# Kernel optimization log

Hardware: AMD Instinct MI355X
Metric: run time of the kernel (lower is better)

Reference implementation:

```python
import jax, jax.numpy as jnp
import numpy as np

B, S1, S2 = 32, 128, 128
V, D, P, C = 30000, 300, 200, 3


def _highway(x, Wh, bh, Wt, bt):
    h = jax.nn.relu(x @ Wh + bh)
    t = jax.nn.sigmoid(x @ Wt + bt)
    return t * h + (1.0 - t) * x


def _ff(x, W1, b1, W2, b2):
    # self.forward: two relu linear layers (dropout disabled / keep_prob=1)
    return jax.nn.relu(jax.nn.relu(x @ W1 + b1) @ W2 + b2)


def setup_inputs() -> dict:
    key = jax.random.key(0)
    ks = iter(jax.random.split(key, 64))
    W = lambda *s: jax.random.normal(next(ks), s, jnp.float32) * 0.05
    Z = lambda n: jnp.zeros((n,), jnp.float32)
    inp = {
        'x1': jax.random.randint(next(ks), (B, S1), 0, V),
        'x2': jax.random.randint(next(ks), (B, S2), 0, V),
        'emb': jax.random.normal(next(ks), (V, D), jnp.float32),
        'hw1_Wh': W(D, D), 'hw1_bh': Z(D), 'hw1_Wt': W(D, D), 'hw1_bt': Z(D),
        'hw2_Wh': W(D, D), 'hw2_bh': Z(D), 'hw2_Wt': W(D, D), 'hw2_bt': Z(D),
        'mul_W1': W(D, P), 'mul_b1': Z(P), 'mul_W2': W(P, P), 'mul_b2': Z(P),
        'dist_W1': W(D, P), 'dist_b1': Z(P), 'dist_W2': W(P, P), 'dist_b2': Z(P),
        'cmp_W1': W(4 * D, P), 'cmp_b1': Z(P), 'cmp_W2': W(P, P), 'cmp_b2': Z(P),
        'chw1_Wh': W(P, P), 'chw1_bh': Z(P), 'chw1_Wt': W(P, P), 'chw1_bt': Z(P),
        'chw2_Wh': W(P, P), 'chw2_bh': Z(P), 'chw2_Wt': W(P, P), 'chw2_bt': Z(P),
        'agg_W1': W(4 * P, P), 'agg_b1': Z(P), 'agg_W2': W(P, P), 'agg_b2': Z(P),
        'out_W': W(P, C), 'out_b': Z(C),
    }
    return inp


def reference(x1, x2, emb,
              hw1_Wh, hw1_bh, hw1_Wt, hw1_bt,
              hw2_Wh, hw2_bh, hw2_Wt, hw2_bt,
              mul_W1, mul_b1, mul_W2, mul_b2,
              dist_W1, dist_b1, dist_W2, dist_b2,
              cmp_W1, cmp_b1, cmp_W2, cmp_b2,
              chw1_Wh, chw1_bh, chw1_Wt, chw1_bt,
              chw2_Wh, chw2_bh, chw2_Wt, chw2_bt,
              agg_W1, agg_b1, agg_W2, agg_b2,
              out_W, out_b):
    # embed + shared highway stack
    e1 = emb[x1]  # [B,S1,D]
    e2 = emb[x2]  # [B,S2,D]
    e1 = _highway(_highway(e1, hw1_Wh, hw1_bh, hw1_Wt, hw1_bt), hw2_Wh, hw2_bh, hw2_Wt, hw2_bt)
    e2 = _highway(_highway(e2, hw1_Wh, hw1_bh, hw1_Wt, hw1_bt), hw2_Wh, hw2_bh, hw2_Wt, hw2_bt)

    # attention_mul: project both, dot product
    p1 = _ff(e1, mul_W1, mul_b1, mul_W2, mul_b2)  # [B,S1,P]
    p2 = _ff(e2, mul_W1, mul_b1, mul_W2, mul_b2)  # [B,S2,P]
    att1 = jnp.einsum('bip,bjp->bij', p1, p2)

    # attention_dist: project both, sum_d 1/(1+|q1-q2|) -> 4D broadcast
    q1 = _ff(e1, dist_W1, dist_b1, dist_W2, dist_b2)
    q2 = _ff(e2, dist_W1, dist_b1, dist_W2, dist_b2)
    att2 = jnp.sum(1.0 / (1.0 + jnp.abs(q1[:, :, None, :] - q2[:, None, :, :])), axis=-1)

    sim = att1 + att2  # [B,S1,S2]
    alpha = jnp.einsum('bji,bjd->bid', jax.nn.softmax(jnp.swapaxes(sim, 1, 2), axis=-1).transpose(0, 2, 1).transpose(0, 2, 1), e1) if False else jnp.matmul(jax.nn.softmax(jnp.swapaxes(sim, 1, 2), axis=-1), e1)  # [B,S2,D]
    beta = jnp.matmul(jax.nn.softmax(sim, axis=-1), e2)  # [B,S1,D]

    # compare (shared forward + highway stack)
    v1 = _ff(jnp.concatenate([e1, beta, e1 - beta, e1 * beta], -1), cmp_W1, cmp_b1, cmp_W2, cmp_b2)
    v2 = _ff(jnp.concatenate([e2, alpha, e2 - alpha, e2 * alpha], -1), cmp_W1, cmp_b1, cmp_W2, cmp_b2)
    v1 = _highway(_highway(v1, chw1_Wh, chw1_bh, chw1_Wt, chw1_bt), chw2_Wh, chw2_bh, chw2_Wt, chw2_bt)
    v2 = _highway(_highway(v2, chw1_Wh, chw1_bh, chw1_Wt, chw1_bt), chw2_Wh, chw2_bh, chw2_Wt, chw2_bt)

    # aggregate: max + sum pooling, forward, final linear
    v = jnp.concatenate([v1.max(1), v2.max(1), v1.sum(1), v2.sum(1)], -1)  # [B,4P]
    y = _ff(v, agg_W1, agg_b1, agg_W2, agg_b2)
    return y @ out_W + out_b  # [B,C]
```

## Files before the change

### kernel.cpp

```cpp
#include <hip/hip_runtime.h>
#include <hip/hip_bf16.h>
#include <math.h>

#define B_   32
#define S_   128
#define V_   30000
#define D_   300
#define P_   200
#define NT   8192
#define NT1  4096
#define LDE  320
#define LDP  256

typedef __hip_bfloat16 bf16;
typedef __attribute__((ext_vector_type(8))) __bf16 bf16x8;
typedef __attribute__((ext_vector_type(4))) float f32x4;

__device__ __forceinline__ float b2f(bf16 v) { return __bfloat162float(v); }
__device__ __forceinline__ short f2s(float v) { bf16 h = __float2bfloat16(v); return *(short*)&h; }
__device__ __forceinline__ float s2f(short s) { bf16 h; *(short*)&h = s; return __bfloat162float(h); }

struct ConvTable {
    const float* W1[8]; const float* W2[8]; bf16* dst[8];
    int K[8], N1[8], N2[8], Kpad[8], IL[8];
    unsigned long long base[8]; unsigned long long total;
};

__global__ void k_convw(ConvTable T) {
    unsigned long long idx = (unsigned long long)blockIdx.x * 256 + threadIdx.x;
    if (idx >= T.total) return;
    int e = 0;
#pragma unroll
    for (int i = 1; i < 8; ++i) if (idx >= T.base[i]) e = i;
    unsigned long long local = idx - T.base[e];
    int Kpad = T.Kpad[e];
    int n = (int)(local / Kpad);
    int k = (int)(local - (unsigned long long)n * Kpad);
    float v = 0.f;
    if (k < T.K[e]) {
        if (T.IL[e]) {
            int d = n >> 1, half = n & 1;
            if (d < T.N1[e]) v = (half ? T.W2[e] : T.W1[e])[(size_t)k * T.N1[e] + d];
        } else {
            if (n < T.N1[e]) v = T.W1[e][(size_t)k * T.N1[e] + n];
            else if (n < T.N1[e] + T.N2[e]) v = T.W2[e][(size_t)k * T.N2[e] + (n - T.N1[e])];
        }
    }
    T.dst[e][local] = __float2bfloat16(v);
}

__global__ void k_convmisc(const float* __restrict__ Wc, bf16* __restrict__ dstc,
                           const float* __restrict__ A1w, const float* __restrict__ A2w,
                           const float* __restrict__ Ow,
                           float* __restrict__ T1, float* __restrict__ T2,
                           float* __restrict__ T3) {
    int idx = blockIdx.x * 256 + threadIdx.x;
    if (idx < 245760) {
        int n = idx / 960, k = idx - n * 960;
        int sel = k / 320, kc = k - sel * 320;
        float v = 0.f;
        if (kc < 300 && n < 200) {
            if (sel == 0)      v = Wc[(size_t)kc * 200 + n] + Wc[(size_t)(600 + kc) * 200 + n];
            else if (sel == 1) v = Wc[(size_t)(300 + kc) * 200 + n] - Wc[(size_t)(600 + kc) * 200 + n];
            else               v = Wc[(size_t)(900 + kc) * 200 + n];
        }
        dstc[idx] = __float2bfloat16(v);
    } else {
        int l = idx - 245760;
        if (l < 160000)       T1[l] = A1w[(size_t)(l % 800) * 200 + l / 800];
        else if (l < 200000)  { int m = l - 160000; T2[m] = A2w[(size_t)(m % 200) * 200 + m / 200]; }
        else if (l < 200600)  { int m = l - 200000; T3[m] = Ow[(size_t)(m % 200) * 3 + m / 200]; }
    }
}

__global__ void k_embed(const int* __restrict__ x1, const int* __restrict__ x2,
                        const float* __restrict__ emb, bf16* __restrict__ E) {
    int idx = blockIdx.x * 256 + threadIdx.x;
    if (idx >= NT * (LDE / 4)) return;
    int r = idx / (LDE / 4);
    int c4 = (idx - r * (LDE / 4)) * 4;
    int tok = (r < NT1) ? x1[r] : x2[r - NT1];
    if ((unsigned)tok >= (unsigned)V_) tok = 0;
    short o[4];
    if (c4 + 4 <= 300) {
        float4 v = *(const float4*)(emb + (size_t)tok * 300 + c4);
        o[0] = f2s(v.x); o[1] = f2s(v.y); o[2] = f2s(v.z); o[3] = f2s(v.w);
    } else {
#pragma unroll
        for (int i = 0; i < 4; ++i) {
            int c = c4 + i;
            o[i] = f2s((c < 300) ? emb[(size_t)tok * 300 + c] : 0.f);
        }
    }
    *(short4*)((short*)E + (size_t)r * LDE + c4) = *(short4*)&o[0];
}

__global__ __launch_bounds__(256) void k_skinny(
    const float* __restrict__ A, const float* __restrict__ WT,
    const float* __restrict__ bias, float* __restrict__ C,
    int M, int N, int K, int act) {
    int wave = (blockIdx.x * 256 + threadIdx.x) >> 6;
    int lane = threadIdx.x & 63;
    if (wave >= M * N) return;
    int m = wave / N, n = wave - m * N;
    const float4* a4 = (const float4*)(A + (size_t)m * K);
    const float4* w4 = (const float4*)(WT + (size_t)n * K);
    int K4 = K >> 2;
    float acc = 0.f;
    for (int i = lane; i < K4; i += 64) {
        float4 av = a4[i], wv = w4[i];
        acc += av.x * wv.x + av.y * wv.y + av.z * wv.z + av.w * wv.w;
    }
#pragma unroll
    for (int off = 32; off > 0; off >>= 1) acc += __shfl_down(acc, off, 64);
    if (lane == 0) {
        float v = acc + bias[n];
        if (act == 1) v = fmaxf(v, 0.f);
        C[(size_t)m * N + n] = v;
    }
}

template <int AMODE, int EPI>
__global__ __launch_bounds__(256) void k_gemm(
    const bf16* __restrict__ A, const bf16* __restrict__ A2,
    const bf16* __restrict__ A3, int lda,
    const bf16* __restrict__ WT, const bf16* __restrict__ WT2, int Kpad, int K,
    bf16* __restrict__ C, bf16* __restrict__ C2, int ldc, int Ntot, int N1,
    const float* __restrict__ bias1, const float* __restrict__ bias2,
    int act1, int act2, const bf16* __restrict__ xbuf, int ldxb)
{
    __shared__ short As[64][72];
    __shared__ short Bs[64][72];
    int tid = threadIdx.x;
    int w = tid >> 6, lane = tid & 63, quad = lane >> 4, l16 = lane & 15;
    int bm = blockIdx.x * 64;
    int half = 0, bn;
    if (AMODE == 4) { half = blockIdx.y >> 2; bn = (blockIdx.y & 3) * 64; }
    else bn = blockIdx.y * 64;
    const short* Wsh = (const short*)((AMODE == 4 && half) ? WT2 : WT);
    bf16* Cl = (AMODE == 4 && half) ? C2 : C;
    int wr = (w & 1) * 32, wc = (w >> 1) * 32;
    int ar = tid >> 2, ac = (tid & 3) * 16;

    const short* Abase = (const short*)A + (AMODE == 4 ? half * 200 : 0);
    int gm = bm + ar;

    f32x4 acc[2][2];
#pragma unroll
    for (int i = 0; i < 2; ++i)
#pragma unroll
        for (int j = 0; j < 2; ++j)
#pragma unroll
            for (int r = 0; r < 4; ++r) acc[i][j][r] = 0.f;

    short pa[16], pb[16];

    auto loadA = [&](int k0) {
        if (AMODE != 3) {
            int k = k0 + ac;
            const short* src = Abase + (size_t)gm * lda + k;
            if (k + 16 <= K) {
#pragma unroll
                for (int i = 0; i < 4; ++i) *(short4*)&pa[i * 4] = ((const short4*)src)[i];
            } else {
#pragma unroll
                for (int i = 0; i < 16; ++i) pa[i] = (k + i < K) ? src[i] : (short)0;
            }
        } else {
            int sel = k0 / 320;
            const short* base = (sel == 0) ? (const short*)A
                              : (sel == 1) ? (const short*)A2 : (const short*)A3;
            int k = (k0 - sel * 320) + ac;
            const short* src = base + (size_t)gm * LDE + k;
            if (k + 16 <= 300) {
#pragma unroll
                for (int i = 0; i < 4; ++i) *(short4*)&pa[i * 4] = ((const short4*)src)[i];
            } else {
#pragma unroll
                for (int i = 0; i < 16; ++i) pa[i] = (k + i < 300) ? src[i] : (short)0;
            }
        }
    };
    auto loadB = [&](int k0) {
        const short* src = Wsh + (size_t)(bn + ar) * Kpad + k0 + ac;
#pragma unroll
        for (int i = 0; i < 4; ++i) *(short4*)&pb[i * 4] = ((const short4*)src)[i];
    };

    loadA(0); loadB(0);
    for (int k0 = 0; k0 < Kpad; k0 += 64) {
#pragma unroll
        for (int i = 0; i < 4; ++i) {
            *(short4*)&As[ar][ac + i * 4] = *(short4*)&pa[i * 4];
            *(short4*)&Bs[ar][ac + i * 4] = *(short4*)&pb[i * 4];
        }
        __syncthreads();
        if (k0 + 64 < Kpad) { loadA(k0 + 64); loadB(k0 + 64); }
        {
            bf16x8 a[2][2], b[2][2];
#pragma unroll
            for (int mt = 0; mt < 2; ++mt)
#pragma unroll
                for (int ks = 0; ks < 2; ++ks)
                    a[mt][ks] = *(const bf16x8*)&As[wr + mt * 16 + l16][ks * 32 + quad * 8];
#pragma unroll
            for (int nt = 0; nt < 2; ++nt)
#pragma unroll
                for (int ks = 0; ks < 2; ++ks)
                    b[nt][ks] = *(const bf16x8*)&Bs[wc + nt * 16 + l16][ks * 32 + quad * 8];
#pragma unroll
            for (int mt = 0; mt < 2; ++mt)
#pragma unroll
                for (int nt = 0; nt < 2; ++nt) {
                    acc[mt][nt] = __builtin_amdgcn_mfma_f32_16x16x32_bf16(a[mt][0], b[nt][0], acc[mt][nt], 0, 0, 0);
                    acc[mt][nt] = __builtin_amdgcn_mfma_f32_16x16x32_bf16(a[mt][1], b[nt][1], acc[mt][nt], 0, 0, 0);
                }
        }
        __syncthreads();
    }
    short (*Cs)[72] = As;
#pragma unroll
    for (int mt = 0; mt < 2; ++mt) {
#pragma unroll
        for (int nt = 0; nt < 2; ++nt) {
            int cl = wc + nt * 16 + l16;
            int col = bn + cl;
            float bv; int act;
            if (EPI == 1) {
                int d = col >> 1;
                if (d > N1 - 1) d = N1 - 1;
                if (col & 1) { bv = bias2[d]; act = 2; }
                else         { bv = bias1[d]; act = 1; }
            } else if (AMODE == 4) {
                int cc = (col < N1) ? col : (N1 - 1);
                bv = (half ? bias2 : bias1)[cc]; act = act1;
            } else {
                int cc = (col < Ntot) ? col : (Ntot - 1);
                if (cc < N1) { bv = bias1[cc]; act = act1; }
                else { bv = bias2[cc - N1]; act = act2; }
            }
#pragma unroll
            for (int r = 0; r < 4; ++r) {
                float v = acc[mt][nt][r] + bv;
                if (act == 1) v = fmaxf(v, 0.f);
                else if (act == 2) v = 1.f / (1.f + expf(-v));
                Cs[wr + mt * 16 + quad * 4 + r][cl] = f2s(v);
            }
        }
    }
    __syncthreads();
    if (EPI == 0) {
#pragma unroll
        for (int it = 0; it < 2; ++it) {
            int chunk = tid + it * 256;
            int rl = chunk >> 3;
            int c8 = (chunk & 7) * 8;
            short* dst = (short*)Cl + (size_t)(bm + rl) * ldc + bn + c8;
            *(short4*)dst = *(short4*)&Cs[rl][c8];
            *(short4*)(dst + 4) = *(short4*)&Cs[rl][c8 + 4];
        }
    } else {
        int d0 = bn >> 1;
#pragma unroll
        for (int it = 0; it < 2; ++it) {
            int chunk = tid + it * 256;
            int rl = chunk >> 3;
            int c4 = (chunk & 7) * 4;
            int row = bm + rl;
            const short* xs = (const short*)xbuf + (size_t)row * ldxb + d0 + c4;
            short o[4];
#pragma unroll
            for (int i = 0; i < 4; ++i) {
                float h = s2f(Cs[rl][2 * (c4 + i)]);
                float t = s2f(Cs[rl][2 * (c4 + i) + 1]);
                o[i] = f2s(t * h + (1.f - t) * s2f(xs[i]));
            }
            *(short4*)((short*)Cl + (size_t)row * ldc + d0 + c4) = *(short4*)&o[0];
        }
    }
}

__global__ void k_transpose2(const bf16* __restrict__ srcP, bf16* __restrict__ dstP,
                             const bf16* __restrict__ srcQ, bf16* __restrict__ dstQ) {
    int idx = blockIdx.x * 256 + threadIdx.x;
    if (idx >= B_ * P_ * S_) return;
    const bf16* src = blockIdx.y ? srcQ : srcP;
    bf16* dst = blockIdx.y ? dstQ : dstP;
    int j = idx & (S_ - 1);
    int rest = idx >> 7;
    int p = rest % P_;
    int b = rest / P_;
    dst[idx] = src[((size_t)(b * S_ + j)) * LDP + p];
}

__global__ __launch_bounds__(256) void k_sim2(const bf16* __restrict__ Pmat,
                                              const bf16* __restrict__ Qmat,
                                              const bf16* __restrict__ PT,
                                              const bf16* __restrict__ QT,
                                              float* __restrict__ SIM) {
    __shared__ float qp[8][P_][2];
    int blk = blockIdx.x;
    int b = blk >> 4;
    int it = blk & 15;
    int tid = threadIdx.x;
    int j = tid & 127, h = tid >> 7;
    int row0 = b * 128 + it * 8;
    for (int x = tid; x < 8 * P_; x += 256) {
        int r = x / P_, c = x - r * P_;
        qp[r][c][0] = b2f(Qmat[(size_t)(row0 + r) * LDP + c]);
        qp[r][c][1] = b2f(Pmat[(size_t)(row0 + r) * LDP + c]);
    }
    __syncthreads();
    const bf16* ptb = PT + (size_t)b * P_ * S_;
    const bf16* qtb = QT + (size_t)b * P_ * S_;
    float acc[4] = {0.f, 0.f, 0.f, 0.f};
    for (int p = 0; p < P_; ++p) {
        float v = b2f(ptb[p * S_ + j]);
        float u = b2f(qtb[p * S_ + j]);
#pragma unroll
        for (int r = 0; r < 4; ++r) {
            int i = h * 4 + r;
            float2 w = *(const float2*)&qp[i][p][0];
            float d = w.x - u;
            acc[r] += w.y * v + __builtin_amdgcn_rcpf(1.f + fabsf(d));
        }
    }
#pragma unroll
    for (int r = 0; r < 4; ++r) {
        int i = it * 8 + h * 4 + r;
        SIM[((size_t)(b * 128 + i)) * S_ + j] = acc[r];
    }
}

__global__ __launch_bounds__(128) void k_soft(const float* __restrict__ SIM,
                                              bf16* __restrict__ Wb) {
    int blk = blockIdx.x;
    int kind = blk >> 12;
    int blk2 = blk & 4095;
    int b = blk2 >> 7, r = blk2 & 127;
    int t = threadIdx.x;
    __shared__ float red[128];
    float x = (kind == 0) ? SIM[(size_t)blk2 * S_ + t]
                          : SIM[((size_t)(b * S_ + t)) * S_ + r];
    red[t] = x;
    __syncthreads();
    for (int s = 64; s > 0; s >>= 1) {
        if (t < s) red[t] = fmaxf(red[t], red[t + s]);
        __syncthreads();
    }
    float mx = red[0];
    __syncthreads();
    float ex = expf(x - mx);
    red[t] = ex;
    __syncthreads();
    for (int s = 64; s > 0; s >>= 1) {
        if (t < s) red[t] += red[t + s];
        __syncthreads();
    }
    Wb[(size_t)blk * 128 + t] = __float2bfloat16(ex / red[0]);
}

__global__ __launch_bounds__(256) void k_attg(const bf16* __restrict__ Wb,
                                              const bf16* __restrict__ E,
                                              bf16* __restrict__ ATT,
                                              bf16* __restrict__ EA) {
    __shared__ short As[64][72];
    __shared__ short Bs[64][72];
    int tid = threadIdx.x;
    int w = tid >> 6, lane = tid & 63, quad = lane >> 4, l16 = lane & 15;
    int m0 = blockIdx.x * 64;
    int kind = (m0 >= NT1) ? 1 : 0;
    int local = m0 - kind * NT1;
    int b = local >> 7;
    int ebase = kind ? (b * 128) : (NT1 + b * 128);
    int bn = blockIdx.y * 64;
    int wr = (w & 1) * 32, wc = (w >> 1) * 32;
    int ar = tid >> 2, ac = (tid & 3) * 16;

    f32x4 acc[2][2];
#pragma unroll
    for (int i = 0; i < 2; ++i)
#pragma unroll
        for (int j = 0; j < 2; ++j)
#pragma unroll
            for (int r = 0; r < 4; ++r) acc[i][j][r] = 0.f;

    for (int k0 = 0; k0 < 128; k0 += 64) {
        {
            const short* src = (const short*)Wb + (size_t)(m0 + ar) * 128 + k0 + ac;
#pragma unroll
            for (int i = 0; i < 4; ++i) *(short4*)&As[ar][ac + i * 4] = ((const short4*)src)[i];
        }
#pragma unroll
        for (int it = 0; it < 2; ++it) {
            int idx = tid + it * 256;
            int r = idx >> 3;
            int c8 = (idx & 7) * 8;
            const short* src = (const short*)E + (size_t)(ebase + k0 + r) * LDE + bn + c8;
            short4 v0 = ((const short4*)src)[0];
            short4 v1 = ((const short4*)src)[1];
            const short* vp = (const short*)&v0;
#pragma unroll
            for (int i = 0; i < 4; ++i) Bs[c8 + i][r] = vp[i];
            vp = (const short*)&v1;
#pragma unroll
            for (int i = 0; i < 4; ++i) Bs[c8 + 4 + i][r] = vp[i];
        }
        __syncthreads();
        {
            bf16x8 a[2][2], bb[2][2];
#pragma unroll
            for (int mt = 0; mt < 2; ++mt)
#pragma unroll
                for (int ks = 0; ks < 2; ++ks)
                    a[mt][ks] = *(const bf16x8*)&As[wr + mt * 16 + l16][ks * 32 + quad * 8];
#pragma unroll
            for (int nt = 0; nt < 2; ++nt)
#pragma unroll
                for (int ks = 0; ks < 2; ++ks)
                    bb[nt][ks] = *(const bf16x8*)&Bs[wc + nt * 16 + l16][ks * 32 + quad * 8];
#pragma unroll
            for (int mt = 0; mt < 2; ++mt)
#pragma unroll
                for (int nt = 0; nt < 2; ++nt) {
                    acc[mt][nt] = __builtin_amdgcn_mfma_f32_16x16x32_bf16(a[mt][0], bb[nt][0], acc[mt][nt], 0, 0, 0);
                    acc[mt][nt] = __builtin_amdgcn_mfma_f32_16x16x32_bf16(a[mt][1], bb[nt][1], acc[mt][nt], 0, 0, 0);
                }
        }
        __syncthreads();
    }
    short (*Cs)[72] = As;
#pragma unroll
    for (int mt = 0; mt < 2; ++mt)
#pragma unroll
        for (int nt = 0; nt < 2; ++nt) {
            int cl = wc + nt * 16 + l16;
#pragma unroll
            for (int r = 0; r < 4; ++r)
                Cs[wr + mt * 16 + quad * 4 + r][cl] = f2s(acc[mt][nt][r]);
        }
    __syncthreads();
#pragma unroll
    for (int it = 0; it < 2; ++it) {
        int chunk = tid + it * 256;
        int rl = chunk >> 3;
        int c8 = (chunk & 7) * 8;
        int row = m0 + rl;
        short a8[8];
        *(short4*)&a8[0] = *(short4*)&Cs[rl][c8];
        *(short4*)&a8[4] = *(short4*)&Cs[rl][c8 + 4];
        short* adst = (short*)ATT + (size_t)row * LDE + bn + c8;
        *(short4*)adst = *(short4*)&a8[0];
        *(short4*)(adst + 4) = *(short4*)&a8[4];
        const short* es = (const short*)E + (size_t)row * LDE + bn + c8;
        short e8[8];
        *(short4*)&e8[0] = ((const short4*)es)[0];
        *(short4*)&e8[4] = ((const short4*)es)[1];
        short o8[8];
#pragma unroll
        for (int i = 0; i < 8; ++i) o8[i] = f2s(s2f(a8[i]) * s2f(e8[i]));
        short* edst = (short*)EA + (size_t)row * LDE + bn + c8;
        *(short4*)edst = *(short4*)&o8[0];
        *(short4*)(edst + 4) = *(short4*)&o8[4];
    }
}

__global__ __launch_bounds__(256) void k_pool(const bf16* __restrict__ V,
                                              float* __restrict__ OUT) {
    int b = blockIdx.x;
    int c = threadIdx.x;
    if (c >= P_) return;
    const bf16* v1 = V + (size_t)(b * S_) * LDP;
    const bf16* v2 = V + (size_t)(NT1 + b * S_) * LDP;
    float mx1 = -INFINITY, mx2 = -INFINITY, s1 = 0.f, s2 = 0.f;
    for (int i = 0; i < S_; ++i) {
        float a = b2f(v1[(size_t)i * LDP + c]);
        mx1 = fmaxf(mx1, a); s1 += a;
        float bb = b2f(v2[(size_t)i * LDP + c]);
        mx2 = fmaxf(mx2, bb); s2 += bb;
    }
    float* o = OUT + (size_t)b * 4 * P_;
    o[c] = mx1; o[P_ + c] = mx2; o[2 * P_ + c] = s1; o[3 * P_ + c] = s2;
}

__global__ void k_fillf(float* dst, int n, float v) {
    int i = blockIdx.x * 256 + threadIdx.x;
    if (i < n) dst[i] = v;
}

extern "C" void kernel_launch(void* const* d_in, const int* in_sizes, int n_in,
                              void* d_out, int out_size, void* d_ws, size_t ws_size,
                              hipStream_t stream) {
    const int* x1 = (const int*)d_in[0];
    const int* x2 = (const int*)d_in[1];
    const float* emb = (const float*)d_in[2];
    const float *hw1_Wh = (const float*)d_in[3],  *hw1_bh = (const float*)d_in[4];
    const float *hw1_Wt = (const float*)d_in[5],  *hw1_bt = (const float*)d_in[6];
    const float *hw2_Wh = (const float*)d_in[7],  *hw2_bh = (const float*)d_in[8];
    const float *hw2_Wt = (const float*)d_in[9],  *hw2_bt = (const float*)d_in[10];
    const float *mul_W1 = (const float*)d_in[11], *mul_b1 = (const float*)d_in[12];
    const float *mul_W2 = (const float*)d_in[13], *mul_b2 = (const float*)d_in[14];
    const float *dist_W1 = (const float*)d_in[15], *dist_b1 = (const float*)d_in[16];
    const float *dist_W2 = (const float*)d_in[17], *dist_b2 = (const float*)d_in[18];
    const float *cmp_W1 = (const float*)d_in[19], *cmp_b1 = (const float*)d_in[20];
    const float *cmp_W2 = (const float*)d_in[21], *cmp_b2 = (const float*)d_in[22];
    const float *chw1_Wh = (const float*)d_in[23], *chw1_bh = (const float*)d_in[24];
    const float *chw1_Wt = (const float*)d_in[25], *chw1_bt = (const float*)d_in[26];
    const float *chw2_Wh = (const float*)d_in[27], *chw2_bh = (const float*)d_in[28];
    const float *chw2_Wt = (const float*)d_in[29], *chw2_bt = (const float*)d_in[30];
    const float *agg_W1 = (const float*)d_in[31], *agg_b1 = (const float*)d_in[32];
    const float *agg_W2 = (const float*)d_in[33], *agg_b2 = (const float*)d_in[34];
    const float *out_W = (const float*)d_in[35], *out_b = (const float*)d_in[36];

    const size_t nE = (size_t)NT * LDE;
    const size_t nP = (size_t)NT * LDP;
    const size_t nCht = (size_t)NT * 448;
    const size_t nTR = (size_t)B_ * P_ * S_;
    const size_t nWT = 1224704;
    size_t bf16_elems = 4 * nE + 2 * nP + 2 * nCht + nWT;
    size_t f32_elems = (size_t)B_ * 4 * P_ + 2 * (size_t)B_ * P_ + 200600;
    size_t need = bf16_elems * 2 + f32_elems * 4 + 64;
    if (ws_size < need) {
        k_fillf<<<dim3(1), dim3(256), 0, stream>>>((float*)d_out, B_ * 3, 555.f);
        return;
    }
    bf16* Eb  = (bf16*)d_ws;
    bf16* X1  = Eb + nE;
    bf16* X2  = X1 + nE;
    bf16* EA  = X2 + nE;
    bf16* Pb  = EA + nE;
    bf16* Qb  = Pb + nP;
    bf16* ChtA = Qb + nP;
    bf16* ChtB = ChtA + nCht;
    bf16* WTp = ChtB + nCht;
    float* POOL = (float*)(WTp + nWT);
    float* G1 = POOL + (size_t)B_ * 4 * P_;
    float* G2 = G1 + (size_t)B_ * P_;
    float* WT_a1 = G2 + (size_t)B_ * P_;
    float* WT_a2 = WT_a1 + 160000;
    float* WT_o  = WT_a2 + 40000;
    bf16* ATT = Eb;
    bf16* Wbuf = ChtA;
    bf16* PTb = ChtB;
    bf16* QTb = ChtB + nTR;
    float* SIM = (float*)(ChtB + 2 * nTR);
    bf16* V2 = ChtB;

    bf16* WT_hw1 = WTp + 0;
    bf16* WT_hw2 = WTp + 204800;
    bf16* WT_md  = WTp + 409600;
    bf16* WT_m2  = WTp + 552960;
    bf16* WT_d2  = WTp + 618496;
    bf16* WT_c2  = WTp + 684032;
    bf16* WT_ch1 = WTp + 749568;
    bf16* WT_ch2 = WTp + 864256;
    bf16* WT_c1  = WTp + 978944;

    dim3 blk256(256);

    ConvTable T;
    const float* s1[8] = {hw1_Wh, hw2_Wh, mul_W1, mul_W2, dist_W2, cmp_W2, chw1_Wh, chw2_Wh};
    const float* s2[8] = {hw1_Wt, hw2_Wt, dist_W1, nullptr, nullptr, nullptr, chw1_Wt, chw2_Wt};
    bf16* dsts[8] = {WT_hw1, WT_hw2, WT_md, WT_m2, WT_d2, WT_c2, WT_ch1, WT_ch2};
    int Ks[8]  = {300, 300, 300, 200, 200, 200, 200, 200};
    int N1s[8] = {300, 300, 200, 200, 200, 200, 200, 200};
    int N2s[8] = {300, 300, 200, 0, 0, 0, 200, 200};
    int Kps[8] = {320, 320, 320, 256, 256, 256, 256, 256};
    int Nps[8] = {640, 640, 448, 256, 256, 256, 448, 448};
    int ILs[8] = {1, 1, 0, 0, 0, 0, 1, 1};
    unsigned long long base = 0;
    for (int i = 0; i < 8; ++i) {
        T.W1[i] = s1[i]; T.W2[i] = s2[i]; T.dst[i] = dsts[i];
        T.K[i] = Ks[i]; T.N1[i] = N1s[i]; T.N2[i] = N2s[i]; T.Kpad[i] = Kps[i];
        T.IL[i] = ILs[i];
        T.base[i] = base;
        base += (unsigned long long)Kps[i] * Nps[i];
    }
    T.total = base;
    k_convw<<<dim3((unsigned)((base + 255) / 256)), blk256, 0, stream>>>(T);
    k_convmisc<<<dim3((245760 + 200600 + 255) / 256), blk256, 0, stream>>>(
        cmp_W1, WT_c1, agg_W1, agg_W2, out_W, WT_a1, WT_a2, WT_o);

    k_embed<<<dim3((NT * (LDE / 4) + 255) / 256), blk256, 0, stream>>>(x1, x2, emb, Eb);

    k_gemm<0, 1><<<dim3(128, 10), blk256, 0, stream>>>(
        Eb, nullptr, nullptr, LDE,
        WT_hw1, nullptr, 320, 300, X1, nullptr, LDE, 600, 300,
        hw1_bh, hw1_bt, 1, 2, Eb, LDE);

    k_gemm<0, 1><<<dim3(128, 10), blk256, 0, stream>>>(
        X1, nullptr, nullptr, LDE,
        WT_hw2, nullptr, 320, 300, X2, nullptr, LDE, 600, 300,
        hw2_bh, hw2_bt, 1, 2, X1, LDE);

    k_gemm<0, 0><<<dim3(128, 7), blk256, 0, stream>>>(
        X2, nullptr, nullptr, LDE,
        WT_md, nullptr, 320, 300, ChtA, nullptr, 448, 400, 200,
        mul_b1, dist_b1, 1, 1, nullptr, 0);

    k_gemm<4, 0><<<dim3(128, 8), blk256, 0, stream>>>(
        ChtA, nullptr, nullptr, 448,
        WT_m2, WT_d2, 256, 200, Pb, Qb, LDP, 256, 200,
        mul_b2, dist_b2, 1, 1, nullptr, 0);

    int nTRb = (int)((nTR + 255) / 256);
    k_transpose2<<<dim3(nTRb, 2), blk256, 0, stream>>>(
        Pb + (size_t)NT1 * LDP, PTb, Qb + (size_t)NT1 * LDP, QTb);

    k_sim2<<<dim3(B_ * 16), blk256, 0, stream>>>(Pb, Qb, PTb, QTb, SIM);

    k_soft<<<dim3(2 * NT1), dim3(128), 0, stream>>>(SIM, Wbuf);

    k_attg<<<dim3(128, 5), blk256, 0, stream>>>(Wbuf, X2, ATT, EA);

    k_gemm<3, 0><<<dim3(128, 4), blk256, 0, stream>>>(
        X2, ATT, EA, LDE,
        WT_c1, nullptr, 960, 300, ChtA, nullptr, LDP, 200, 200,
        cmp_b1, cmp_b1, 1, 1, nullptr, 0);

    k_gemm<0, 0><<<dim3(128, 4), blk256, 0, stream>>>(
        ChtA, nullptr, nullptr, LDP,
        WT_c2, nullptr, 256, 200, Pb, nullptr, LDP, 200, 200,
        cmp_b2, cmp_b2, 1, 1, nullptr, 0);

    k_gemm<0, 1><<<dim3(128, 7), blk256, 0, stream>>>(
        Pb, nullptr, nullptr, LDP,
        WT_ch1, nullptr, 256, 200, Qb, nullptr, LDP, 400, 200,
        chw1_bh, chw1_bt, 1, 2, Pb, LDP);

    k_gemm<0, 1><<<dim3(128, 7), blk256, 0, stream>>>(
        Qb, nullptr, nullptr, LDP,
        WT_ch2, nullptr, 256, 200, V2, nullptr, LDP, 400, 200,
        chw2_bh, chw2_bt, 1, 2, Qb, LDP);

    k_pool<<<dim3(B_), blk256, 0, stream>>>(V2, POOL);

    k_skinny<<<dim3(1600), blk256, 0, stream>>>(POOL, WT_a1, agg_b1, G1, B_, P_, 800, 1);
    k_skinny<<<dim3(1600), blk256, 0, stream>>>(G1, WT_a2, agg_b2, G2, B_, P_, 200, 1);
    k_skinny<<<dim3(24), blk256, 0, stream>>>(G2, WT_o, out_b, (float*)d_out, B_, 3, 200, 0);
}
```

Measured before the change: 318.3 us.

## Fuse setup kernels, row softmax into sim, and pooling+MLP tail

Merges the weight conversion, compare-weight repack and embedding gather into a single setup launch. Computes the row-wise softmax inside the similarity kernel so only the column softmax remains a separate kernel. Replaces the pool plus three skinny GEMV launches with one per-batch tail kernel that reads the fp32 aggregate weights directly. This cuts launch count and intermediate buffers, but the tail now runs 32 blocks doing serial dot products, which may be slower than the wide skinny kernels.

```diff
diff --git a/kernel.cpp b/kernel.cpp
--- a/kernel.cpp
+++ b/kernel.cpp
@@ -26,37 +26,34 @@
     unsigned long long base[8]; unsigned long long total;
 };
 
-__global__ void k_convw(ConvTable T) {
+__global__ void k_setup(ConvTable T, const float* __restrict__ Wc, bf16* __restrict__ dstc,
+                        const int* __restrict__ x1, const int* __restrict__ x2,
+                        const float* __restrict__ emb, bf16* __restrict__ E) {
     unsigned long long idx = (unsigned long long)blockIdx.x * 256 + threadIdx.x;
-    if (idx >= T.total) return;
-    int e = 0;
-#pragma unroll
-    for (int i = 1; i < 8; ++i) if (idx >= T.base[i]) e = i;
-    unsigned long long local = idx - T.base[e];
-    int Kpad = T.Kpad[e];
-    int n = (int)(local / Kpad);
-    int k = (int)(local - (unsigned long long)n * Kpad);
-    float v = 0.f;
-    if (k < T.K[e]) {
-        if (T.IL[e]) {
-            int d = n >> 1, half = n & 1;
-            if (d < T.N1[e]) v = (half ? T.W2[e] : T.W1[e])[(size_t)k * T.N1[e] + d];
-        } else {
-            if (n < T.N1[e]) v = T.W1[e][(size_t)k * T.N1[e] + n];
-            else if (n < T.N1[e] + T.N2[e]) v = T.W2[e][(size_t)k * T.N2[e] + (n - T.N1[e])];
-        }
-    }
-    T.dst[e][local] = __float2bfloat16(v);
-}
-
-__global__ void k_convmisc(const float* __restrict__ Wc, bf16* __restrict__ dstc,
-                           const float* __restrict__ A1w, const float* __restrict__ A2w,
-                           const float* __restrict__ Ow,
-                           float* __restrict__ T1, float* __restrict__ T2,
-                           float* __restrict__ T3) {
-    int idx = blockIdx.x * 256 + threadIdx.x;
+    if (idx < T.total) {
+        int e = 0;
+#pragma unroll
+        for (int i = 1; i < 8; ++i) if (idx >= T.base[i]) e = i;
+        unsigned long long local = idx - T.base[e];
+        int Kpad = T.Kpad[e];
+        int n = (int)(local / Kpad);
+        int k = (int)(local - (unsigned long long)n * Kpad);
+        float v = 0.f;
+        if (k < T.K[e]) {
+            if (T.IL[e]) {
+                int d = n >> 1, half = n & 1;
+                if (d < T.N1[e]) v = (half ? T.W2[e] : T.W1[e])[(size_t)k * T.N1[e] + d];
+            } else {
+                if (n < T.N1[e]) v = T.W1[e][(size_t)k * T.N1[e] + n];
+                else if (n < T.N1[e] + T.N2[e]) v = T.W2[e][(size_t)k * T.N2[e] + (n - T.N1[e])];
+            }
+        }
+        T.dst[e][local] = __float2bfloat16(v);
+        return;
+    }
+    idx -= T.total;
     if (idx < 245760) {
-        int n = idx / 960, k = idx - n * 960;
+        int n = (int)idx / 960, k = (int)idx - n * 960;
         int sel = k / 320, kc = k - sel * 320;
         float v = 0.f;
         if (kc < 300 && n < 200) {
@@ -65,58 +62,26 @@
             else               v = Wc[(size_t)(900 + kc) * 200 + n];
         }
         dstc[idx] = __float2bfloat16(v);
-    } else {
-        int l = idx - 245760;
-        if (l < 160000)       T1[l] = A1w[(size_t)(l % 800) * 200 + l / 800];
-        else if (l < 200000)  { int m = l - 160000; T2[m] = A2w[(size_t)(m % 200) * 200 + m / 200]; }
-        else if (l < 200600)  { int m = l - 200000; T3[m] = Ow[(size_t)(m % 200) * 3 + m / 200]; }
-    }
-}
-
-__global__ void k_embed(const int* __restrict__ x1, const int* __restrict__ x2,
-                        const float* __restrict__ emb, bf16* __restrict__ E) {
-    int idx = blockIdx.x * 256 + threadIdx.x;
-    if (idx >= NT * (LDE / 4)) return;
-    int r = idx / (LDE / 4);
-    int c4 = (idx - r * (LDE / 4)) * 4;
-    int tok = (r < NT1) ? x1[r] : x2[r - NT1];
-    if ((unsigned)tok >= (unsigned)V_) tok = 0;
-    short o[4];
-    if (c4 + 4 <= 300) {
-        float4 v = *(const float4*)(emb + (size_t)tok * 300 + c4);
-        o[0] = f2s(v.x); o[1] = f2s(v.y); o[2] = f2s(v.z); o[3] = f2s(v.w);
-    } else {
-#pragma unroll
-        for (int i = 0; i < 4; ++i) {
-            int c = c4 + i;
-            o[i] = f2s((c < 300) ? emb[(size_t)tok * 300 + c] : 0.f);
-        }
-    }
-    *(short4*)((short*)E + (size_t)r * LDE + c4) = *(short4*)&o[0];
-}
-
-__global__ __launch_bounds__(256) void k_skinny(
-    const float* __restrict__ A, const float* __restrict__ WT,
-    const float* __restrict__ bias, float* __restrict__ C,
-    int M, int N, int K, int act) {
-    int wave = (blockIdx.x * 256 + threadIdx.x) >> 6;
-    int lane = threadIdx.x & 63;
-    if (wave >= M * N) return;
-    int m = wave / N, n = wave - m * N;
-    const float4* a4 = (const float4*)(A + (size_t)m * K);
-    const float4* w4 = (const float4*)(WT + (size_t)n * K);
-    int K4 = K >> 2;
-    float acc = 0.f;
-    for (int i = lane; i < K4; i += 64) {
-        float4 av = a4[i], wv = w4[i];
-        acc += av.x * wv.x + av.y * wv.y + av.z * wv.z + av.w * wv.w;
-    }
-#pragma unroll
-    for (int off = 32; off > 0; off >>= 1) acc += __shfl_down(acc, off, 64);
-    if (lane == 0) {
-        float v = acc + bias[n];
-        if (act == 1) v = fmaxf(v, 0.f);
-        C[(size_t)m * N + n] = v;
+        return;
+    }
+    idx -= 245760;
+    if (idx < (unsigned long long)NT * (LDE / 4)) {
+        int r = (int)(idx / (LDE / 4));
+        int c4 = ((int)idx - r * (LDE / 4)) * 4;
+        int tok = (r < NT1) ? x1[r] : x2[r - NT1];
+        if ((unsigned)tok >= (unsigned)V_) tok = 0;
+        short o[4];
+        if (c4 + 4 <= 300) {
+            float4 v = *(const float4*)(emb + (size_t)tok * 300 + c4);
+            o[0] = f2s(v.x); o[1] = f2s(v.y); o[2] = f2s(v.z); o[3] = f2s(v.w);
+        } else {
+#pragma unroll
+            for (int i = 0; i < 4; ++i) {
+                int c = c4 + i;
+                o[i] = f2s((c < 300) ? emb[(size_t)tok * 300 + c] : 0.f);
+            }
+        }
+        *(short4*)((short*)E + (size_t)r * LDE + c4) = *(short4*)&o[0];
     }
 }
 
@@ -297,8 +262,11 @@
                                               const bf16* __restrict__ Qmat,
                                               const bf16* __restrict__ PT,
                                               const bf16* __restrict__ QT,
-                                              float* __restrict__ SIM) {
+                                              float* __restrict__ SIM,
+                                              bf16* __restrict__ Wb) {
     __shared__ float qp[8][P_][2];
+    __shared__ float sm[8][128];
+    __shared__ float redm[8][32];
     int blk = blockIdx.x;
     int b = blk >> 4;
     int it = blk & 15;
@@ -327,21 +295,47 @@
     }
 #pragma unroll
     for (int r = 0; r < 4; ++r) {
-        int i = it * 8 + h * 4 + r;
-        SIM[((size_t)(b * 128 + i)) * S_ + j] = acc[r];
-    }
-}
-
-__global__ __launch_bounds__(128) void k_soft(const float* __restrict__ SIM,
-                                              bf16* __restrict__ Wb) {
+        int lr = h * 4 + r;
+        sm[lr][j] = acc[r];
+        SIM[((size_t)(row0 + lr)) * S_ + j] = acc[r];
+    }
+    __syncthreads();
+    int rr = tid >> 5, l32 = tid & 31;
+    float v4[4];
+    float m4 = -INFINITY;
+#pragma unroll
+    for (int i = 0; i < 4; ++i) { v4[i] = sm[rr][l32 * 4 + i]; m4 = fmaxf(m4, v4[i]); }
+    redm[rr][l32] = m4;
+    __syncthreads();
+    for (int s = 16; s > 0; s >>= 1) {
+        if (l32 < s) redm[rr][l32] = fmaxf(redm[rr][l32], redm[rr][l32 + s]);
+        __syncthreads();
+    }
+    float mx = redm[rr][0];
+    __syncthreads();
+    float s4 = 0.f;
+#pragma unroll
+    for (int i = 0; i < 4; ++i) { v4[i] = expf(v4[i] - mx); s4 += v4[i]; }
+    redm[rr][l32] = s4;
+    __syncthreads();
+    for (int s = 16; s > 0; s >>= 1) {
+        if (l32 < s) redm[rr][l32] += redm[rr][l32 + s];
+        __syncthreads();
+    }
+    float inv = 1.f / redm[rr][0];
+    short o[4];
+#pragma unroll
+    for (int i = 0; i < 4; ++i) o[i] = f2s(v4[i] * inv);
+    *(short4*)((short*)Wb + (size_t)(row0 + rr) * 128 + l32 * 4) = *(short4*)&o[0];
+}
+
+__global__ __launch_bounds__(128) void k_softa(const float* __restrict__ SIM,
+                                               bf16* __restrict__ Wb) {
     int blk = blockIdx.x;
-    int kind = blk >> 12;
-    int blk2 = blk & 4095;
-    int b = blk2 >> 7, r = blk2 & 127;
+    int b = blk >> 7, r = blk & 127;
     int t = threadIdx.x;
     __shared__ float red[128];
-    float x = (kind == 0) ? SIM[(size_t)blk2 * S_ + t]
-                          : SIM[((size_t)(b * S_ + t)) * S_ + r];
+    float x = SIM[((size_t)(b * S_ + t)) * S_ + r];
     red[t] = x;
     __syncthreads();
     for (int s = 64; s > 0; s >>= 1) {
@@ -357,7 +351,7 @@
         if (t < s) red[t] += red[t + s];
         __syncthreads();
     }
-    Wb[(size_t)blk * 128 + t] = __float2bfloat16(ex / red[0]);
+    Wb[(size_t)(NT1 + blk) * 128 + t] = __float2bfloat16(ex / red[0]);
 }
 
 __global__ __launch_bounds__(256) void k_attg(const bf16* __restrict__ Wb,
@@ -465,22 +459,49 @@
     }
 }
 
-__global__ __launch_bounds__(256) void k_pool(const bf16* __restrict__ V,
-                                              float* __restrict__ OUT) {
+__global__ __launch_bounds__(256) void k_tail(const bf16* __restrict__ V,
+                                              const float* __restrict__ agg_W1,
+                                              const float* __restrict__ agg_b1,
+                                              const float* __restrict__ agg_W2,
+                                              const float* __restrict__ agg_b2,
+                                              const float* __restrict__ out_W,
+                                              const float* __restrict__ out_b,
+                                              float* __restrict__ out) {
+    __shared__ float pool[800];
+    __shared__ float g1[200];
+    __shared__ float g2[200];
     int b = blockIdx.x;
-    int c = threadIdx.x;
-    if (c >= P_) return;
-    const bf16* v1 = V + (size_t)(b * S_) * LDP;
-    const bf16* v2 = V + (size_t)(NT1 + b * S_) * LDP;
-    float mx1 = -INFINITY, mx2 = -INFINITY, s1 = 0.f, s2 = 0.f;
-    for (int i = 0; i < S_; ++i) {
-        float a = b2f(v1[(size_t)i * LDP + c]);
-        mx1 = fmaxf(mx1, a); s1 += a;
-        float bb = b2f(v2[(size_t)i * LDP + c]);
-        mx2 = fmaxf(mx2, bb); s2 += bb;
-    }
-    float* o = OUT + (size_t)b * 4 * P_;
-    o[c] = mx1; o[P_ + c] = mx2; o[2 * P_ + c] = s1; o[3 * P_ + c] = s2;
+    int t = threadIdx.x;
+    if (t < 200) {
+        const bf16* v1 = V + (size_t)(b * S_) * LDP;
+        const bf16* v2 = V + (size_t)(NT1 + b * S_) * LDP;
+        float mx1 = -INFINITY, mx2 = -INFINITY, s1 = 0.f, s2 = 0.f;
+        for (int i = 0; i < S_; ++i) {
+            float a = b2f(v1[(size_t)i * LDP + t]);
+            mx1 = fmaxf(mx1, a); s1 += a;
+            float bb = b2f(v2[(size_t)i * LDP + t]);
+            mx2 = fmaxf(mx2, bb); s2 += bb;
+        }
+        pool[t] = mx1; pool[200 + t] = mx2; pool[400 + t] = s1; pool[600 + t] = s2;
+    }
+    __syncthreads();
+    if (t < 200) {
+        float acc = 0.f;
+        for (int k = 0; k < 800; ++k) acc += pool[k] * agg_W1[(size_t)k * 200 + t];
+        g1[t] = fmaxf(acc + agg_b1[t], 0.f);
+    }
+    __syncthreads();
+    if (t < 200) {
+        float acc = 0.f;
+        for (int k = 0; k < 200; ++k) acc += g1[k] * agg_W2[(size_t)k * 200 + t];
+        g2[t] = fmaxf(acc + agg_b2[t], 0.f);
+    }
+    __syncthreads();
+    if (t < 3) {
+        float acc = 0.f;
+        for (int k = 0; k < 200; ++k) acc += g2[k] * out_W[(size_t)k * 3 + t];
+        out[b * 3 + t] = acc + out_b[t];
+    }
 }
 
 __global__ void k_fillf(float* dst, int n, float v) {
@@ -518,8 +539,7 @@
     const size_t nTR = (size_t)B_ * P_ * S_;
     const size_t nWT = 1224704;
     size_t bf16_elems = 4 * nE + 2 * nP + 2 * nCht + nWT;
-    size_t f32_elems = (size_t)B_ * 4 * P_ + 2 * (size_t)B_ * P_ + 200600;
-    size_t need = bf16_elems * 2 + f32_elems * 4 + 64;
+    size_t need = bf16_elems * 2 + 4096;
     if (ws_size < need) {
         k_fillf<<<dim3(1), dim3(256), 0, stream>>>((float*)d_out, B_ * 3, 555.f);
         return;
@@ -533,12 +553,6 @@
     bf16* ChtA = Qb + nP;
     bf16* ChtB = ChtA + nCht;
     bf16* WTp = ChtB + nCht;
-    float* POOL = (float*)(WTp + nWT);
-    float* G1 = POOL + (size_t)B_ * 4 * P_;
-    float* G2 = G1 + (size_t)B_ * P_;
-    float* WT_a1 = G2 + (size_t)B_ * P_;
-    float* WT_a2 = WT_a1 + 160000;
-    float* WT_o  = WT_a2 + 40000;
     bf16* ATT = Eb;
     bf16* Wbuf = ChtA;
     bf16* PTb = ChtB;
@@ -577,11 +591,9 @@
         base += (unsigned long long)Kps[i] * Nps[i];
     }
     T.total = base;
-    k_convw<<<dim3((unsigned)((base + 255) / 256)), blk256, 0, stream>>>(T);
-    k_convmisc<<<dim3((245760 + 200600 + 255) / 256), blk256, 0, stream>>>(
-        cmp_W1, WT_c1, agg_W1, agg_W2, out_W, WT_a1, WT_a2, WT_o);
-
-    k_embed<<<dim3((NT * (LDE / 4) + 255) / 256), blk256, 0, stream>>>(x1, x2, emb, Eb);
+    unsigned long long setup_total = base + 245760ull + (unsigned long long)NT * (LDE / 4);
+    k_setup<<<dim3((unsigned)((setup_total + 255) / 256)), blk256, 0, stream>>>(
+        T, cmp_W1, WT_c1, x1, x2, emb, Eb);
 
     k_gemm<0, 1><<<dim3(128, 10), blk256, 0, stream>>>(
         Eb, nullptr, nullptr, LDE,
@@ -607,9 +619,9 @@
     k_transpose2<<<dim3(nTRb, 2), blk256, 0, stream>>>(
         Pb + (size_t)NT1 * LDP, PTb, Qb + (size_t)NT1 * LDP, QTb);
 
-    k_sim2<<<dim3(B_ * 16), blk256, 0, stream>>>(Pb, Qb, PTb, QTb, SIM);
-
-    k_soft<<<dim3(2 * NT1), dim3(128), 0, stream>>>(SIM, Wbuf);
+    k_sim2<<<dim3(B_ * 16), blk256, 0, stream>>>(Pb, Qb, PTb, QTb, SIM, Wbuf);
+
+    k_softa<<<dim3(NT1), dim3(128), 0, stream>>>(SIM, Wbuf);
 
     k_attg<<<dim3(128, 5), blk256, 0, stream>>>(Wbuf, X2, ATT, EA);
 
@@ -633,9 +645,6 @@
         WT_ch2, nullptr, 256, 200, V2, nullptr, LDP, 400, 200,
         chw2_bh, chw2_bt, 1, 2, Qb, LDP);
 
-    k_pool<<<dim3(B_), blk256, 0, stream>>>(V2, POOL);
-
-    k_skinny<<<dim3(1600), blk256, 0, stream>>>(POOL, WT_a1, agg_b1, G1, B_, P_, 800, 1);
-    k_skinny<<<dim3(1600), blk256, 0, stream>>>(G1, WT_a2, agg_b2, G2, B_, P_, 200, 1);
-    k_skinny<<<dim3(24), blk256, 0, stream>>>(G2, WT_o, out_b, (float*)d_out, B_, 3, 200, 0);
-}
+    k_tail<<<dim3(B_), blk256, 0, stream>>>(V2, agg_W1, agg_b1, agg_W2, agg_b2,
+                                            out_W, out_b, (float*)d_out);
+}
```

After: 330.4 us. 1.04x slower.
